# Performance work log

Measured on AMD Instinct MI355X. Metric: run time of the kernel, lower is better.

## Reference

```python
import jax, jax.numpy as jnp
import numpy as np

NEG = -1e9

def gat_layer(x, edge_mask, W, al, ar, rW, b, act):
    # x: (B, N, Fin); edge_mask: (B, N, N) bool, edge u->v at [b,u,v]
    B, N, _ = x.shape
    H, D = al.shape
    f = (x @ W).reshape(B, N, H, D)                      # (B,N,H,D)
    el = jnp.einsum('bnhd,hd->bnh', f, al)               # src term
    er = jnp.einsum('bnhd,hd->bnh', f, ar)               # dst term
    # e[b,u,v,h] = LeakyReLU(el[src=u] + er[dst=v]), slope 0.2 (dgl default)
    e = jax.nn.leaky_relu(el[:, :, None, :] + er[:, None, :, :], 0.2)
    logits = jnp.where(edge_mask[..., None], e, NEG)
    # masked, empty-column-safe softmax over incoming edges (axis=1 = src u)
    m = jnp.max(logits, axis=1, keepdims=True)
    p = jnp.exp(logits - m) * edge_mask[..., None]
    alpha = p / jnp.clip(jnp.sum(p, axis=1, keepdims=True), 1e-9)
    out = jnp.einsum('buvh,buhd->bvhd', alpha, f)        # scatter-sum to dst
    res = (x @ rW).reshape(B, N, H, D)                   # residual projection
    out = out + res + b.reshape(H, D)
    return act(out) if act is not None else out


def setup_inputs() -> dict:
    key = jax.random.key(0)
    ks = jax.random.split(key, 12)
    n, c, h, w = 16, 64, 32, 32
    num_s, hid, H = 64, 64, 4
    seg = jax.random.normal(ks[0], (n, c, h, w), dtype=jnp.float32)
    adj = jax.random.normal(ks[1], (n, h * w, h * w), dtype=jnp.float32)
    s = 0.1
    return {
        'seg': seg, 'adj': adj,
        'W0': jax.random.normal(ks[2], (num_s, H * hid), dtype=jnp.float32) * s,
        'al0': jax.random.normal(ks[3], (H, hid), dtype=jnp.float32) * s,
        'ar0': jax.random.normal(ks[4], (H, hid), dtype=jnp.float32) * s,
        'rW0': jax.random.normal(ks[5], (num_s, H * hid), dtype=jnp.float32) * s,
        'b0': jnp.zeros((H * hid,), dtype=jnp.float32),
        'W1': jax.random.normal(ks[6], (H * hid, H * num_s), dtype=jnp.float32) * s,
        'al1': jax.random.normal(ks[7], (H, num_s), dtype=jnp.float32) * s,
        'ar1': jax.random.normal(ks[8], (H, num_s), dtype=jnp.float32) * s,
        'rW1': jax.random.normal(ks[9], (H * hid, H * num_s), dtype=jnp.float32) * s,
        'b1': jnp.zeros((H * num_s,), dtype=jnp.float32),
    }


def reference(seg, adj, W0, al0, ar0, rW0, b0, W1, al1, ar1, rW1, b1):
    n, c, h, w = seg.shape
    num_s = W0.shape[0]
    x = seg.reshape(n, -1, num_s)                        # (n, N, num_s)
    k = (h * w) // 6
    topv, _ = jax.lax.top_k(adj, k)
    thr = topv[..., -1]                                  # k-th largest per row
    adj_t = jnp.where(adj >= thr[..., None], adj, 0.0)
    edge_mask = adj_t > 0                                # (n, N, N)
    fea = gat_layer(x, edge_mask, W0, al0, ar0, rW0, b0, jax.nn.elu)
    fea = fea.reshape(n, fea.shape[1], -1)               # flatten heads
    fea = gat_layer(fea, edge_mask, W1, al1, ar1, rW1, b1, None)
    out = fea.mean(axis=2)                               # mean over heads -> (n, N, num_s)
    return out.reshape(n, -1, num_s)
```

## Files before the change

### kernel.cpp

```cpp
#include <hip/hip_runtime.h>
#include <hip/hip_bf16.h>
#include <stdint.h>

#define BB   16
#define NN   1024
#define KSEL 170
#define LOG2E 1.4426950408889634f

typedef __attribute__((ext_vector_type(8))) short short8;
typedef __attribute__((ext_vector_type(4))) short short4v;
typedef __attribute__((ext_vector_type(4))) float f32x4;

static __device__ __forceinline__ short f2bf(float x) {
    __hip_bfloat16 h = __float2bfloat16(x);
    return *reinterpret_cast<short*>(&h);
}
static __device__ __forceinline__ float bf2f(short x) {
    uint32_t u = ((uint32_t)(uint16_t)x) << 16;
    return __uint_as_float(u);
}
static __device__ __forceinline__ float fast_exp2(float x) {
    float r; asm("v_exp_f32 %0, %1" : "=v"(r) : "v"(x)); return r;
}

__global__ __launch_bounds__(256) void k_topk_mask(
    const float* __restrict__ adj, uint64_t* __restrict__ mask)
{
    const int wid = threadIdx.x >> 6, lane = threadIdx.x & 63;
    const int row = blockIdx.x * 4 + wid;
    const float* a = adj + (size_t)row * NN;
    __shared__ uint32_t hist[4][256];
    uint32_t* h = hist[wid];

    uint32_t key[16];
    #pragma unroll
    for (int j = 0; j < 16; ++j) {
        uint32_t u = __float_as_uint(a[lane + j * 64]);
        key[j] = u ^ ((u >> 31) ? 0xFFFFFFFFu : 0x80000000u);
    }

    uint32_t prefix = 0u, kk = KSEL;
    #pragma unroll
    for (int pass = 0; pass < 2; ++pass) {
        const int shift = 24 - 8 * pass;
        const uint32_t hi_mask = pass ? 0xFF000000u : 0u;
        *(uint4*)&h[lane * 4] = make_uint4(0u, 0u, 0u, 0u);
        __builtin_amdgcn_wave_barrier();
        #pragma unroll
        for (int j = 0; j < 16; ++j)
            if ((key[j] & hi_mask) == prefix)
                atomicAdd(&h[(key[j] >> shift) & 255], 1u);
        __builtin_amdgcn_wave_barrier();
        const uint4 c4 = *(const uint4*)&h[lane * 4];
        const uint32_t T = c4.x + c4.y + c4.z + c4.w;
        uint32_t s = T;
        #pragma unroll
        for (int off = 1; off < 64; off <<= 1) {
            uint32_t v = __shfl_down(s, off);
            s += (lane + off < 64) ? v : 0u;
        }
        const uint32_t E = s - T;
        const uint32_t s3 = c4.w;
        const uint32_t s2 = c4.z + s3;
        const uint32_t s1 = c4.y + s2;
        const uint32_t s0 = c4.x + s1;
        const uint32_t ci[4] = {c4.x, c4.y, c4.z, c4.w};
        const uint32_t si[4] = {s0, s1, s2, s3};
        uint32_t found = 0u, nb = 0u, nk = 0u;
        #pragma unroll
        for (int i = 0; i < 4; ++i) {
            uint32_t incl = E + si[i];
            uint32_t excl = incl - ci[i];
            if (excl < kk && kk <= incl) { found = 1u; nb = (uint32_t)(lane * 4 + i); nk = kk - excl; }
        }
        uint64_t bal = __ballot(found != 0u);
        int wl = __ffsll((unsigned long long)bal) - 1;
        prefix = prefix | ((uint32_t)__shfl((int)nb, wl) << shift);
        kk = (uint32_t)__shfl((int)nk, wl);
    }

    uint32_t sv[16];
    #pragma unroll
    for (int j = 0; j < 16; ++j)
        sv[j] = ((key[j] ^ prefix) >> 16) == 0u ? key[j] : 0u;

    uint32_t thr_key;
    for (;;) {
        uint32_t m = 0u;
        #pragma unroll
        for (int j = 0; j < 16; ++j) m = m > sv[j] ? m : sv[j];
        #pragma unroll
        for (int off = 1; off < 64; off <<= 1) {
            uint32_t v = __shfl_xor(m, off);
            m = m > v ? m : v;
        }
        if (m == 0u) { thr_key = 0u; break; }
        uint32_t c = 0u;
        #pragma unroll
        for (int j = 0; j < 16; ++j) c += (sv[j] == m) ? 1u : 0u;
        #pragma unroll
        for (int off = 1; off < 64; off <<= 1)
            c += __shfl_xor(c, off);
        if (kk <= c) { thr_key = m; break; }
        kk -= c;
        #pragma unroll
        for (int j = 0; j < 16; ++j) if (sv[j] == m) sv[j] = 0u;
    }

    #pragma unroll
    for (int j = 0; j < 16; ++j) {
        bool pred = (key[j] >= thr_key) && (key[j] > 0x80000000u);
        uint64_t bal = __ballot(pred);
        if (lane == 0) mask[(size_t)row * 16 + j] = bal;
    }
}

__global__ __launch_bounds__(256) void k_maskT(
    const uint64_t* __restrict__ mask, uint64_t* __restrict__ maskT)
{
    const int tile = blockIdx.x * 4 + (threadIdx.x >> 6);
    const int lane = threadIdx.x & 63;
    const int b  = tile >> 8;
    const int uw = (tile >> 4) & 15;
    const int vw = tile & 15;
    const size_t bN = (size_t)b * NN;
    uint64_t w = mask[(bN + uw * 64 + lane) * 16 + vw];
    uint64_t r_out = 0;
    #pragma unroll
    for (int j = 0; j < 64; ++j) {
        uint64_t r = __ballot((w >> j) & 1ull);
        if (lane == j) r_out = r;
    }
    maskT[(bN + vw * 64 + lane) * 16 + uw] = r_out;
}

__global__ __launch_bounds__(256) void k_prepare(
    const float* __restrict__ W0, const float* __restrict__ rW0,
    const float* __restrict__ W1, const float* __restrict__ rW1,
    const float* __restrict__ seg,
    short* __restrict__ Wt0, short* __restrict__ rWt0,
    short* __restrict__ Wt1, short* __restrict__ rWt1,
    short* __restrict__ xb0)
{
    const int bid = blockIdx.x, t = threadIdx.x;
    if (bid < 64) {
        int idx = bid * 256 + t;
        int o = idx >> 6, k = idx & 63;
        Wt0[idx] = f2bf(W0[(size_t)k * 256 + o]);
    } else if (bid < 128) {
        int idx = (bid - 64) * 256 + t;
        int o = idx >> 6, k = idx & 63;
        rWt0[idx] = f2bf(rW0[(size_t)k * 256 + o]);
    } else if (bid < 384) {
        int idx = (bid - 128) * 256 + t;
        int o = idx >> 8, k = idx & 255;
        Wt1[idx] = f2bf(W1[(size_t)k * 256 + o]);
    } else if (bid < 640) {
        int idx = (bid - 384) * 256 + t;
        int o = idx >> 8, k = idx & 255;
        rWt1[idx] = f2bf(rW1[(size_t)k * 256 + o]);
    } else {
        int i = ((bid - 640) * 256 + t) * 4;
        float4 v = *(const float4*)(seg + i);
        short4v o4;
        o4[0] = f2bf(v.x); o4[1] = f2bf(v.y); o4[2] = f2bf(v.z); o4[3] = f2bf(v.w);
        *(short4v*)(xb0 + i) = o4;
    }
}

template<int K>
__global__ __launch_bounds__(256, 2) void k_features_mfma(
    const short* __restrict__ xb,
    const short* __restrict__ Wt,
    const short* __restrict__ rWt,
    const float* __restrict__ al,
    const float* __restrict__ ar,
    short* __restrict__ ft,
    short* __restrict__ fea,
    float* __restrict__ el_t,
    float* __restrict__ er_t)
{
    const int tid = threadIdx.x, lane = tid & 63, hh = tid >> 6;
    const int l15 = lane & 15, l4 = lane >> 4;
    const int n0 = blockIdx.x * 32;
    const int b_idx = n0 >> 10;
    const int nloc = n0 & (NN - 1);
    const int bh = b_idx * 4 + hh;
    const int XP = K + 8;

    __shared__ short x_lds[32 * (K + 8)];

    const int CH = K / 8;
    #pragma unroll
    for (int c = tid; c < 32 * CH; c += 256) {
        const int row = c / CH, col = c - row * CH;
        *(short8*)&x_lds[row * XP + col * 8] =
            *(const short8*)(xb + ((size_t)n0 + row) * K + col * 8);
    }
    __syncthreads();

    const short* wbase = Wt  + (size_t)(hh * 64 + l15) * K + l4 * 8;
    const short* rbase = rWt + (size_t)(hh * 64 + l15) * K + l4 * 8;
    const size_t qs = (size_t)16 * K;

    f32x4 accf[2][4], accr[2][4];
    #pragma unroll
    for (int s = 0; s < 2; ++s)
        #pragma unroll
        for (int q = 0; q < 4; ++q) {
            accf[s][q] = (f32x4){0.f, 0.f, 0.f, 0.f};
            accr[s][q] = (f32x4){0.f, 0.f, 0.f, 0.f};
        }

    short8 bufW[2][4], bufR[2][4];
    #pragma unroll
    for (int q = 0; q < 4; ++q) {
        bufW[0][q] = *(const short8*)(wbase + q * qs);
        bufR[0][q] = *(const short8*)(rbase + q * qs);
    }

    #pragma unroll
    for (int ks = 0; ks < K / 32; ++ks) {
        const int cur = ks & 1, nxt = cur ^ 1;
        if (ks + 1 < K / 32) {
            #pragma unroll
            for (int q = 0; q < 4; ++q) {
                bufW[nxt][q] = *(const short8*)(wbase + q * qs + (ks + 1) * 32);
                bufR[nxt][q] = *(const short8*)(rbase + q * qs + (ks + 1) * 32);
            }
            __builtin_amdgcn_sched_barrier(0);
        }
        short8 x0 = *(const short8*)&x_lds[l15 * XP + ks * 32 + l4 * 8];
        short8 x1 = *(const short8*)&x_lds[(16 + l15) * XP + ks * 32 + l4 * 8];
        #pragma unroll
        for (int q = 0; q < 4; ++q) {
            accf[0][q] = __builtin_amdgcn_mfma_f32_16x16x32_bf16(x0, bufW[cur][q], accf[0][q], 0, 0, 0);
            accf[1][q] = __builtin_amdgcn_mfma_f32_16x16x32_bf16(x1, bufW[cur][q], accf[1][q], 0, 0, 0);
            accr[0][q] = __builtin_amdgcn_mfma_f32_16x16x32_bf16(bufR[cur][q], x0, accr[0][q], 0, 0, 0);
            accr[1][q] = __builtin_amdgcn_mfma_f32_16x16x32_bf16(bufR[cur][q], x1, accr[1][q], 0, 0, 0);
        }
    }

    #pragma unroll
    for (int s = 0; s < 2; ++s) {
        const int nl = nloc + s * 16;
        #pragma unroll
        for (int q = 0; q < 4; ++q) {
            short4v pk;
            #pragma unroll
            for (int r = 0; r < 4; ++r) pk[r] = f2bf(accf[s][q][r]);
            const int dl = q * 16 + l15;
            const size_t idx = ((size_t)bh << 16)
                             + (size_t)(nl >> 6) * 4096
                             + (size_t)(((nl & 63) >> 3) + (l4 >> 1)) * 512
                             + (size_t)dl * 8 + (l4 & 1) * 4;
            *(short4v*)(ft + idx) = pk;
        }
        float elv[4] = {0.f, 0.f, 0.f, 0.f}, erv[4] = {0.f, 0.f, 0.f, 0.f};
        #pragma unroll
        for (int q = 0; q < 4; ++q) {
            const float alv = al[hh * 64 + q * 16 + l15];
            const float arv = ar[hh * 64 + q * 16 + l15];
            #pragma unroll
            for (int r = 0; r < 4; ++r) {
                elv[r] = fmaf(accf[s][q][r], alv, elv[r]);
                erv[r] = fmaf(accf[s][q][r], arv, erv[r]);
            }
        }
        #pragma unroll
        for (int r = 0; r < 4; ++r) {
            #pragma unroll
            for (int off = 1; off < 16; off <<= 1) {
                elv[r] += __shfl_xor(elv[r], off);
                erv[r] += __shfl_xor(erv[r], off);
            }
        }
        if (l15 == 0) {
            float4 e4, r4;
            e4.x = elv[0] * LOG2E; e4.y = elv[1] * LOG2E;
            e4.z = elv[2] * LOG2E; e4.w = elv[3] * LOG2E;
            r4.x = erv[0] * LOG2E; r4.y = erv[1] * LOG2E;
            r4.z = erv[2] * LOG2E; r4.w = erv[3] * LOG2E;
            *(float4*)(el_t + (size_t)bh * NN + nl + l4 * 4) = e4;
            *(float4*)(er_t + (size_t)bh * NN + nl + l4 * 4) = r4;
        }
        #pragma unroll
        for (int q = 0; q < 4; ++q) {
            short4v pk;
            #pragma unroll
            for (int r = 0; r < 4; ++r) pk[r] = f2bf(accr[s][q][r]);
            *(short4v*)(fea + ((size_t)n0 + s * 16 + l15) * 256 + hh * 64 + q * 16 + l4 * 4) = pk;
        }
    }
}

template<int ELU_ON>
__global__ __launch_bounds__(256, 4) void k_attn(
    const short* __restrict__ ft,
    const float* __restrict__ el_t,
    const float* __restrict__ er_t,
    const uint64_t* __restrict__ maskT,
    const float* __restrict__ bias,
    short* fea)
{
    const int id = blockIdx.x;
    const int swz = (id & 7) * 128 + (id >> 3);
    const int b  = swz >> 6;
    const int h  = (swz >> 4) & 3;
    const int vt = swz & 15;
    const int tid = threadIdx.x;
    const int lane = tid & 63, wid = tid >> 6;
    const int l15 = lane & 15, l4 = lane >> 4;
    const int bh = b * 4 + h;
    const size_t bN = (size_t)b * NN;
    const int v0 = vt * 64;

    __shared__ __align__(16) short f_lds[2][4096];
    __shared__ __align__(16) float el_lds[NN];
    __shared__ __align__(16) uint64_t m_lds[64 * 17];
    __shared__ float smax[4];

    const short* gsrc = ft + ((size_t)bh << 16);

    {
        short8 sa = *(const short8*)(gsrc + tid * 8);
        short8 sb = *(const short8*)(gsrc + 2048 + tid * 8);
        float4 ev4 = ((const float4*)(el_t + (size_t)bh * NN))[tid];
        ((float4*)el_lds)[tid] = ev4;
        float m = fmaxf(fmaxf(ev4.x, ev4.y), fmaxf(ev4.z, ev4.w));
        #pragma unroll
        for (int off = 32; off; off >>= 1) m = fmaxf(m, __shfl_xor(m, off));
        if (lane == 0) smax[wid] = m;
        #pragma unroll
        for (int i = 0; i < 4; ++i) {
            int idx = tid + i * 256;
            m_lds[(idx >> 4) * 17 + (idx & 15)] =
                maskT[(bN + v0 + (idx >> 4)) * 16 + (idx & 15)];
        }
        *(short8*)&f_lds[0][tid * 8] = sa;
        *(short8*)&f_lds[0][2048 + tid * 8] = sb;
    }

    const int vlo = wid * 16 + l15;
    const float er_lo = er_t[(size_t)bh * NN + v0 + vlo];

    __syncthreads();

    const float emx = fmaxf(fmaxf(smax[0], smax[1]), fmaxf(smax[2], smax[3]));
    const float e0 = emx + er_lo;
    const float cv_lo = fmaxf(e0, 0.2f * e0);
    const float c1_lo = er_lo - cv_lo, c2_lo = 0.2f * er_lo - cv_lo;

    const uint8_t* mbytes = (const uint8_t*)m_lds;
    const int moff_lo = vlo * 136;

    short8 ones8;
    #pragma unroll
    for (int i = 0; i < 8; ++i) ones8[i] = (short)0x3F80;

    f32x4 accLo[4];
    #pragma unroll
    for (int i = 0; i < 4; ++i) accLo[i] = (f32x4){0.f, 0.f, 0.f, 0.f};
    f32x4 dLo = (f32x4){0.f, 0.f, 0.f, 0.f};

    short8 Ra, Rb;
    #pragma unroll 1
    for (int tt = 0; tt < 16; ++tt) {
        if (tt < 15) {
            Ra = *(const short8*)(gsrc + (tt + 1) * 4096 + tid * 8);
            Rb = *(const short8*)(gsrc + (tt + 1) * 4096 + 2048 + tid * 8);
            __builtin_amdgcn_sched_barrier(0);
        }
        const short* fb = f_lds[tt & 1];
        #pragma unroll
        for (int kc = 0; kc < 2; ++kc) {
            const float* ep = &el_lds[tt * 64 + kc * 32 + l4 * 8];
            float4 ev0 = *(const float4*)ep;
            float4 ev1 = *(const float4*)(ep + 4);
            const float ev[8] = {ev0.x, ev0.y, ev0.z, ev0.w, ev1.x, ev1.y, ev1.z, ev1.w};
            uint32_t mLo = mbytes[moff_lo + tt * 8 + kc * 4 + l4];
            short8 aLo;
            #pragma unroll
            for (int j = 0; j < 8; ++j) {
                float e = ev[j];
                float argL = fmaxf(e + c1_lo, fmaf(0.2f, e, c2_lo));
                float pL = ((mLo >> j) & 1u) ? fast_exp2(argL) : 0.f;
                aLo[j] = f2bf(pL);
            }
            const int fo = (kc * 4 + l4) * 512 + l15 * 8;
            short8 bw0 = *(const short8*)(fb + fo);
            short8 bw1 = *(const short8*)(fb + fo + 128);
            short8 bw2 = *(const short8*)(fb + fo + 256);
            short8 bw3 = *(const short8*)(fb + fo + 384);
            __builtin_amdgcn_s_setprio(1);
            accLo[0] = __builtin_amdgcn_mfma_f32_16x16x32_bf16(aLo, bw0, accLo[0], 0, 0, 0);
            accLo[1] = __builtin_amdgcn_mfma_f32_16x16x32_bf16(aLo, bw1, accLo[1], 0, 0, 0);
            accLo[2] = __builtin_amdgcn_mfma_f32_16x16x32_bf16(aLo, bw2, accLo[2], 0, 0, 0);
            accLo[3] = __builtin_amdgcn_mfma_f32_16x16x32_bf16(aLo, bw3, accLo[3], 0, 0, 0);
            dLo      = __builtin_amdgcn_mfma_f32_16x16x32_bf16(aLo, ones8, dLo, 0, 0, 0);
            __builtin_amdgcn_s_setprio(0);
        }
        if (tt < 15) {
            *(short8*)&f_lds[(tt + 1) & 1][tid * 8] = Ra;
            *(short8*)&f_lds[(tt + 1) & 1][2048 + tid * 8] = Rb;
        }
        __syncthreads();
    }

    float rcpLo[4];
    #pragma unroll
    for (int r = 0; r < 4; ++r)
        rcpLo[r] = 1.f / fmaxf(dLo[r], 1e-9f);
    #pragma unroll
    for (int dt = 0; dt < 4; ++dt) {
        const int d = dt * 16 + l15;
        const float bv = bias[h * 64 + d];
        #pragma unroll
        for (int r = 0; r < 4; ++r) {
            const int vl = v0 + wid * 16 + l4 * 4 + r;
            const size_t rowL = (bN + vl) * 256 + h * 64 + d;
            float ov = accLo[dt][r] * rcpLo[r] + bf2f(fea[rowL]) + bv;
            if (ELU_ON) ov = ov > 0.f ? ov : __expf(ov) - 1.f;
            fea[rowL] = f2bf(ov);
        }
    }
}

__global__ __launch_bounds__(256) void k_headmean(
    const short* __restrict__ fea, float* __restrict__ outp)
{
    int i = blockIdx.x * 256 + threadIdx.x;
    int d = i & 63;
    size_t node = (size_t)(i >> 6);
    const short* p = fea + node * 256;
    outp[i] = 0.25f * (bf2f(p[d]) + bf2f(p[64 + d]) + bf2f(p[128 + d]) + bf2f(p[192 + d]));
}

extern "C" void kernel_launch(void* const* d_in, const int* in_sizes, int n_in,
                              void* d_out, int out_size, void* d_ws, size_t ws_size,
                              hipStream_t stream) {
    const float* seg = (const float*)d_in[0];
    const float* adj = (const float*)d_in[1];
    const float* W0  = (const float*)d_in[2];
    const float* al0 = (const float*)d_in[3];
    const float* ar0 = (const float*)d_in[4];
    const float* rW0 = (const float*)d_in[5];
    const float* b0  = (const float*)d_in[6];
    const float* W1  = (const float*)d_in[7];
    const float* al1 = (const float*)d_in[8];
    const float* ar1 = (const float*)d_in[9];
    const float* rW1 = (const float*)d_in[10];
    const float* b1  = (const float*)d_in[11];
    float* out = (float*)d_out;

    char* ws = (char*)d_ws;
    size_t off = 0;
    uint64_t* mask  = (uint64_t*)ws;
    off += (size_t)BB * NN * 16 * 8;
    uint64_t* maskT = (uint64_t*)(ws + off); off += (size_t)BB * NN * 16 * 8;
    short* ftb = (short*)(ws + off); off += (size_t)BB * 256 * NN * 2;
    short* fea = (short*)(ws + off); off += (size_t)BB * NN * 256 * 2;
    short* xb0 = (short*)(ws + off); off += (size_t)BB * NN * 64 * 2;
    char* r0 = (char*)mask;
    short* Wt0  = (short*)r0;                 r0 += 256 * 64 * 2;
    short* rWt0 = (short*)r0;                 r0 += 256 * 64 * 2;
    short* Wt1  = (short*)r0;                 r0 += 256 * 256 * 2;
    short* rWt1 = (short*)r0;                 r0 += 256 * 256 * 2;
    float* el   = (float*)r0;                 r0 += (size_t)BB * 4 * NN * 4;
    float* er   = (float*)r0;                 r0 += (size_t)BB * 4 * NN * 4;

    k_topk_mask<<<BB * NN / 4, 256, 0, stream>>>(adj, mask);
    k_maskT<<<BB * 256 / 4, 256, 0, stream>>>(mask, maskT);
    k_prepare<<<640 + BB * NN * 64 / 1024, 256, 0, stream>>>(
        W0, rW0, W1, rW1, seg, Wt0, rWt0, Wt1, rWt1, xb0);

    k_features_mfma<64><<<BB * NN / 32, 256, 0, stream>>>(xb0, Wt0, rWt0, al0, ar0,
                                                          ftb, fea, el, er);
    k_attn<1><<<1024, 256, 0, stream>>>(ftb, el, er, maskT, b0, fea);
    k_features_mfma<256><<<BB * NN / 32, 256, 0, stream>>>(fea, Wt1, rWt1, al1, ar1,
                                                           ftb, fea, el, er);
    k_attn<0><<<1024, 256, 0, stream>>>(ftb, el, er, maskT, b1, fea);

    k_headmean<<<BB * NN * 64 / 256, 256, 0, stream>>>(fea, out);
}
```

Measured before the change: 153.4 us.

## Merge mask transpose into prep kernel, pack attention math, vectorize head mean

Folds the mask transpose into the weight/input preparation kernel so one launch replaces two. The weight buffers move out of the mask region into their own workspace slot, since the mask is still being read in the same launch. The attention logit computation is rewritten with two-wide float vectors to encourage packed FP32 instructions. The head-mean kernel now handles eight outputs per thread with vector loads and stores. Together these target launch overhead and instruction count, at the cost of a little extra workspace.

```diff
diff --git a/kernel.cpp b/kernel.cpp
--- a/kernel.cpp
+++ b/kernel.cpp
@@ -10,6 +10,7 @@
 typedef __attribute__((ext_vector_type(8))) short short8;
 typedef __attribute__((ext_vector_type(4))) short short4v;
 typedef __attribute__((ext_vector_type(4))) float f32x4;
+typedef __attribute__((ext_vector_type(2))) float float2v;
 
 static __device__ __forceinline__ short f2bf(float x) {
     __hip_bfloat16 h = __float2bfloat16(x);
@@ -115,26 +116,8 @@
     }
 }
 
-__global__ __launch_bounds__(256) void k_maskT(
-    const uint64_t* __restrict__ mask, uint64_t* __restrict__ maskT)
-{
-    const int tile = blockIdx.x * 4 + (threadIdx.x >> 6);
-    const int lane = threadIdx.x & 63;
-    const int b  = tile >> 8;
-    const int uw = (tile >> 4) & 15;
-    const int vw = tile & 15;
-    const size_t bN = (size_t)b * NN;
-    uint64_t w = mask[(bN + uw * 64 + lane) * 16 + vw];
-    uint64_t r_out = 0;
-    #pragma unroll
-    for (int j = 0; j < 64; ++j) {
-        uint64_t r = __ballot((w >> j) & 1ull);
-        if (lane == j) r_out = r;
-    }
-    maskT[(bN + vw * 64 + lane) * 16 + uw] = r_out;
-}
-
-__global__ __launch_bounds__(256) void k_prepare(
+__global__ __launch_bounds__(256) void k_mask_prep(
+    const uint64_t* __restrict__ mask, uint64_t* __restrict__ maskT,
     const float* __restrict__ W0, const float* __restrict__ rW0,
     const float* __restrict__ W1, const float* __restrict__ rW1,
     const float* __restrict__ seg,
@@ -143,24 +126,39 @@
     short* __restrict__ xb0)
 {
     const int bid = blockIdx.x, t = threadIdx.x;
-    if (bid < 64) {
-        int idx = bid * 256 + t;
+    if (bid < 1024) {
+        const int tile = bid * 4 + (t >> 6);
+        const int lane = t & 63;
+        const int b  = tile >> 8;
+        const int uw = (tile >> 4) & 15;
+        const int vw = tile & 15;
+        const size_t bN = (size_t)b * NN;
+        uint64_t w = mask[(bN + uw * 64 + lane) * 16 + vw];
+        uint64_t r_out = 0;
+        #pragma unroll
+        for (int j = 0; j < 64; ++j) {
+            uint64_t r = __ballot((w >> j) & 1ull);
+            if (lane == j) r_out = r;
+        }
+        maskT[(bN + vw * 64 + lane) * 16 + uw] = r_out;
+    } else if (bid < 1088) {
+        int idx = (bid - 1024) * 256 + t;
         int o = idx >> 6, k = idx & 63;
         Wt0[idx] = f2bf(W0[(size_t)k * 256 + o]);
-    } else if (bid < 128) {
-        int idx = (bid - 64) * 256 + t;
+    } else if (bid < 1152) {
+        int idx = (bid - 1088) * 256 + t;
         int o = idx >> 6, k = idx & 63;
         rWt0[idx] = f2bf(rW0[(size_t)k * 256 + o]);
-    } else if (bid < 384) {
-        int idx = (bid - 128) * 256 + t;
+    } else if (bid < 1408) {
+        int idx = (bid - 1152) * 256 + t;
         int o = idx >> 8, k = idx & 255;
         Wt1[idx] = f2bf(W1[(size_t)k * 256 + o]);
-    } else if (bid < 640) {
-        int idx = (bid - 384) * 256 + t;
+    } else if (bid < 1664) {
+        int idx = (bid - 1408) * 256 + t;
         int o = idx >> 8, k = idx & 255;
         rWt1[idx] = f2bf(rW1[(size_t)k * 256 + o]);
     } else {
-        int i = ((bid - 640) * 256 + t) * 4;
+        int i = ((bid - 1664) * 256 + t) * 4;
         float4 v = *(const float4*)(seg + i);
         short4v o4;
         o4[0] = f2bf(v.x); o4[1] = f2bf(v.y); o4[2] = f2bf(v.z); o4[3] = f2bf(v.w);
@@ -350,6 +348,9 @@
     const float e0 = emx + er_lo;
     const float cv_lo = fmaxf(e0, 0.2f * e0);
     const float c1_lo = er_lo - cv_lo, c2_lo = 0.2f * er_lo - cv_lo;
+    const float2v c1s = {c1_lo, c1_lo};
+    const float2v c2s = {c2_lo, c2_lo};
+    const float2v k02 = {0.2f, 0.2f};
 
     const uint8_t* mbytes = (const uint8_t*)m_lds;
     const int moff_lo = vlo * 136;
@@ -374,18 +375,17 @@
         const short* fb = f_lds[tt & 1];
         #pragma unroll
         for (int kc = 0; kc < 2; ++kc) {
-            const float* ep = &el_lds[tt * 64 + kc * 32 + l4 * 8];
-            float4 ev0 = *(const float4*)ep;
-            float4 ev1 = *(const float4*)(ep + 4);
-            const float ev[8] = {ev0.x, ev0.y, ev0.z, ev0.w, ev1.x, ev1.y, ev1.z, ev1.w};
+            const float2v* ep2 = (const float2v*)&el_lds[tt * 64 + kc * 32 + l4 * 8];
             uint32_t mLo = mbytes[moff_lo + tt * 8 + kc * 4 + l4];
             short8 aLo;
             #pragma unroll
-            for (int j = 0; j < 8; ++j) {
-                float e = ev[j];
-                float argL = fmaxf(e + c1_lo, fmaf(0.2f, e, c2_lo));
-                float pL = ((mLo >> j) & 1u) ? fast_exp2(argL) : 0.f;
-                aLo[j] = f2bf(pL);
+            for (int jj = 0; jj < 4; ++jj) {
+                float2v e2 = ep2[jj];
+                float2v arg = __builtin_elementwise_max(e2 + c1s, e2 * k02 + c2s);
+                float p0 = ((mLo >> (2 * jj)) & 1u)     ? fast_exp2(arg.x) : 0.f;
+                float p1 = ((mLo >> (2 * jj + 1)) & 1u) ? fast_exp2(arg.y) : 0.f;
+                aLo[2 * jj]     = f2bf(p0);
+                aLo[2 * jj + 1] = f2bf(p1);
             }
             const int fo = (kc * 4 + l4) * 512 + l15 * 8;
             short8 bw0 = *(const short8*)(fb + fo);
@@ -429,11 +429,27 @@
 __global__ __launch_bounds__(256) void k_headmean(
     const short* __restrict__ fea, float* __restrict__ outp)
 {
-    int i = blockIdx.x * 256 + threadIdx.x;
-    int d = i & 63;
-    size_t node = (size_t)(i >> 6);
-    const short* p = fea + node * 256;
-    outp[i] = 0.25f * (bf2f(p[d]) + bf2f(p[64 + d]) + bf2f(p[128 + d]) + bf2f(p[192 + d]));
+    const int i = (blockIdx.x * 256 + threadIdx.x) * 8;
+    const int d0 = i & 63;
+    const size_t node = (size_t)(i >> 6);
+    const short* p = fea + node * 256 + d0;
+    short8 h0 = *(const short8*)(p);
+    short8 h1 = *(const short8*)(p + 64);
+    short8 h2 = *(const short8*)(p + 128);
+    short8 h3 = *(const short8*)(p + 192);
+    float4 o0, o1;
+    #pragma unroll
+    for (int j = 0; j < 4; ++j) {
+        float v = 0.25f * (bf2f(h0[j]) + bf2f(h1[j]) + bf2f(h2[j]) + bf2f(h3[j]));
+        (&o0.x)[j] = v;
+    }
+    #pragma unroll
+    for (int j = 0; j < 4; ++j) {
+        float v = 0.25f * (bf2f(h0[4 + j]) + bf2f(h1[4 + j]) + bf2f(h2[4 + j]) + bf2f(h3[4 + j]));
+        (&o1.x)[j] = v;
+    }
+    *(float4*)(outp + i) = o0;
+    *(float4*)(outp + i + 4) = o1;
 }
 
 extern "C" void kernel_launch(void* const* d_in, const int* in_sizes, int n_in,
@@ -461,18 +477,17 @@
     short* ftb = (short*)(ws + off); off += (size_t)BB * 256 * NN * 2;
     short* fea = (short*)(ws + off); off += (size_t)BB * NN * 256 * 2;
     short* xb0 = (short*)(ws + off); off += (size_t)BB * NN * 64 * 2;
+    short* Wt0  = (short*)(ws + off); off += 256 * 64 * 2;
+    short* rWt0 = (short*)(ws + off); off += 256 * 64 * 2;
+    short* Wt1  = (short*)(ws + off); off += 256 * 256 * 2;
+    short* rWt1 = (short*)(ws + off); off += 256 * 256 * 2;
     char* r0 = (char*)mask;
-    short* Wt0  = (short*)r0;                 r0 += 256 * 64 * 2;
-    short* rWt0 = (short*)r0;                 r0 += 256 * 64 * 2;
-    short* Wt1  = (short*)r0;                 r0 += 256 * 256 * 2;
-    short* rWt1 = (short*)r0;                 r0 += 256 * 256 * 2;
     float* el   = (float*)r0;                 r0 += (size_t)BB * 4 * NN * 4;
     float* er   = (float*)r0;                 r0 += (size_t)BB * 4 * NN * 4;
 
     k_topk_mask<<<BB * NN / 4, 256, 0, stream>>>(adj, mask);
-    k_maskT<<<BB * 256 / 4, 256, 0, stream>>>(mask, maskT);
-    k_prepare<<<640 + BB * NN * 64 / 1024, 256, 0, stream>>>(
-        W0, rW0, W1, rW1, seg, Wt0, rWt0, Wt1, rWt1, xb0);
+    k_mask_prep<<<2688, 256, 0, stream>>>(mask, maskT, W0, rW0, W1, rW1, seg,
+                                          Wt0, rWt0, Wt1, rWt1, xb0);
 
     k_features_mfma<64><<<BB * NN / 32, 256, 0, stream>>>(xb0, Wt0, rWt0, al0, ar0,
                                                           ftb, fea, el, er);
@@ -481,5 +496,5 @@
                                                            ftb, fea, el, er);
     k_attn<0><<<1024, 256, 0, stream>>>(ftb, el, er, maskT, b1, fea);
 
-    k_headmean<<<BB * NN * 64 / 256, 256, 0, stream>>>(fea, out);
-}
+    k_headmean<<<BB * NN * 64 / 2048, 256, 0, stream>>>(fea, out);
+}
```

Measured after the change: 150.3 us. 2.0% less time.
